# Kernel optimization log

Measured on AMD Instinct MI355X. Metric: run time of the kernel, lower is better.

Reference implementation:

```python
import jax, jax.numpy as jnp
import numpy as np

B, N, E, D_IN, D_ENC, D_GNN, D_FC, N_CLS = 16, 5000, 160000, 128, 256, 256, 128, 2


def setup_inputs() -> dict:
    key = jax.random.key(0)
    ks = jax.random.split(key, 16)
    sc = lambda d: 1.0 / np.sqrt(d)
    x = jax.random.normal(ks[0], (B, N, D_IN), dtype=jnp.float32)
    edge_index = jax.random.randint(ks[1], (B, 2, E), 0, N, dtype=jnp.int64)
    return {
        "x": x,
        "edge_index": edge_index,
        "We": jax.random.normal(ks[2], (D_IN, D_ENC), jnp.float32) * sc(D_IN),
        "be": jnp.zeros((D_ENC,), jnp.float32),
        "Wl1": jax.random.normal(ks[3], (D_ENC, D_ENC), jnp.float32) * sc(D_ENC),
        "bl1": jnp.zeros((D_ENC,), jnp.float32),
        "Wr1": jax.random.normal(ks[4], (D_ENC, D_ENC), jnp.float32) * sc(D_ENC),
        "Wl2": jax.random.normal(ks[5], (D_ENC, D_GNN), jnp.float32) * sc(D_ENC),
        "bl2": jnp.zeros((D_GNN,), jnp.float32),
        "Wr2": jax.random.normal(ks[6], (D_ENC, D_GNN), jnp.float32) * sc(D_ENC),
        "Wlp": jax.random.normal(ks[7], (D_ENC, 1), jnp.float32) * sc(D_ENC),
        "blp": jnp.zeros((1,), jnp.float32),
        "Wrp": jax.random.normal(ks[8], (D_ENC, 1), jnp.float32) * sc(D_ENC),
        "Wc1": jax.random.normal(ks[9], (D_GNN, D_FC), jnp.float32) * sc(D_GNN),
        "bc1": jnp.zeros((D_FC,), jnp.float32),
        "Wc2": jax.random.normal(ks[10], (D_FC, N_CLS), jnp.float32) * sc(D_FC),
        "bc2": jnp.zeros((N_CLS,), jnp.float32),
    }


def _sage(x, src, dst, Wl, bl, Wr):
    # PyG SAGEConv (mean aggr): lin_l(mean_{j in N(i)} x_j) + lin_r(x_i)
    agg = jax.ops.segment_sum(x[src], dst, num_segments=N)            # [N, d]
    deg = jax.ops.segment_sum(jnp.ones((src.shape[0], 1), x.dtype), dst, num_segments=N)
    mean = agg / jnp.maximum(deg, 1.0)
    return mean @ Wl + bl + x @ Wr


def reference(x, edge_index, We, be, Wl1, bl1, Wr1, Wl2, bl2, Wr2,
              Wlp, blp, Wrp, Wc1, bc1, Wc2, bc2):
    def one_bag(xb, eib):
        src, dst = eib[0], eib[1]
        h = jax.nn.relu(xb @ We + be)                                  # encoder -> [N, d_enc]
        # GNNConvStack (raw_last=False: activation after every layer)
        g = jax.nn.relu(_sage(h, src, dst, Wl1, bl1, Wr1))
        g = jax.nn.relu(_sage(g, src, dst, Wl2, bl2, Wr2))             # [N, d_gnn]
        # pooling SAGEConv on encoder output, softmax over nodes (dim=0)
        cw = jax.nn.softmax(_sage(h, src, dst, Wlp, blp, Wrp), axis=0) # [N, 1]
        # dense_diff_pool re-softmaxes s over clusters (dim=-1); with 1 cluster -> ones
        s = jax.nn.softmax(cw, axis=-1)                                # [N, 1]
        emb = (s.T @ g)[0]                                             # [d_gnn]
        # classifier (raw_last=True)
        h1 = jax.nn.relu(emb @ Wc1 + bc1)
        return h1 @ Wc2 + bc2                                          # [n_classes]

    return jax.vmap(one_bag)(x, edge_index)                           # [B, n_classes]
```

## Files before the change

### kernel.cpp

```cpp
#include <hip/hip_runtime.h>
#include <hip/hip_bf16.h>
#include <cstdint>
#include <cstddef>

#define NBAGS  16
#define NNODES 5000
#define NEDGES 160000
#define DIN    128
#define DENC   256
#define DFC    128
#define NCLS   2

#define TPB 40
#define HB  32
#define HEPB (NEDGES / HB)

typedef __attribute__((ext_vector_type(8))) short short8;
typedef __attribute__((ext_vector_type(4))) float f32x4;

static __device__ __forceinline__ ushort f2b(float v) {
    __hip_bfloat16 b = __float2bfloat16(v);
    return *reinterpret_cast<ushort*>(&b);
}

template<bool DUAL, bool RELU, bool REDUCE>
__global__ __launch_bounds__(256)
void gemm_bf16_kernel(const ushort* __restrict__ A1, const ushort* __restrict__ Wt1,
                      const ushort* __restrict__ A2, const ushort* __restrict__ Wt2,
                      const float* __restrict__ bias, ushort* __restrict__ C,
                      float* __restrict__ emb, int K)
{
    constexpr int LDSP = 40;
    __shared__ __align__(16) ushort As[128 * LDSP];
    __shared__ __align__(16) ushort Bs[128 * LDSP];

    const int bx   = blockIdx.x;
    const int bag  = bx & 15;
    const int rem  = bx >> 4;
    const int col  = rem & 1;
    const int tile = rem >> 1;
    const size_t bagRow0 = (size_t)bag * NNODES;
    const int rloc0 = tile * 128;
    const int n0 = col * 128;

    const int tid  = threadIdx.x;
    const int wave = tid >> 6;
    const int lane = tid & 63;
    const int quad = lane >> 4;
    const int l16  = lane & 15;
    const int wm   = (wave >> 1) * 64;
    const int wn   = (wave & 1) * 64;

    f32x4 acc[4][4];
#pragma unroll
    for (int i = 0; i < 4; ++i)
#pragma unroll
        for (int j = 0; j < 4; ++j)
#pragma unroll
            for (int r = 0; r < 4; ++r) acc[i][j][r] = 0.f;

    const int sr = tid >> 1;
    const int sk = (tid & 1) * 16;

    const int npass = DUAL ? 2 : 1;
    for (int pass = 0; pass < npass; ++pass) {
        const ushort* __restrict__ A = (DUAL && pass) ? A2 : A1;
        const ushort* __restrict__ W = (DUAL && pass) ? Wt2 : Wt1;

        for (int k0 = 0; k0 < K; k0 += 32) {
            {
                uint4 v0 = make_uint4(0, 0, 0, 0), v1 = make_uint4(0, 0, 0, 0);
                const int rl = rloc0 + sr;
                if (rl < NNODES) {
                    const uint4* src = (const uint4*)(A + (bagRow0 + rl) * K + k0 + sk);
                    v0 = src[0]; v1 = src[1];
                }
                *(uint4*)&As[sr * LDSP + sk]     = v0;
                *(uint4*)&As[sr * LDSP + sk + 8] = v1;
            }
            {
                const uint4* src = (const uint4*)(W + (size_t)(n0 + sr) * K + k0 + sk);
                *(uint4*)&Bs[sr * LDSP + sk]     = src[0];
                *(uint4*)&Bs[sr * LDSP + sk + 8] = src[1];
            }
            __syncthreads();

            short8 af[4], bf[4];
#pragma unroll
            for (int t = 0; t < 4; ++t) {
                af[t] = *(const short8*)&As[(wm + t * 16 + l16) * LDSP + quad * 8];
                bf[t] = *(const short8*)&Bs[(wn + t * 16 + l16) * LDSP + quad * 8];
            }
#pragma unroll
            for (int tm = 0; tm < 4; ++tm)
#pragma unroll
                for (int tn = 0; tn < 4; ++tn)
                    acc[tm][tn] = __builtin_amdgcn_mfma_f32_16x16x32_bf16(
                        af[tm], bf[tn], acc[tm][tn], 0, 0, 0);
            __syncthreads();
        }
    }

    if (!REDUCE) {
#pragma unroll
        for (int tm = 0; tm < 4; ++tm) {
            const int rbase = rloc0 + wm + tm * 16 + quad * 4;
#pragma unroll
            for (int reg = 0; reg < 4; ++reg) {
                const int rl = rbase + reg;
                if (rl < NNODES) {
#pragma unroll
                    for (int tn = 0; tn < 4; ++tn) {
                        const int gcol = n0 + wn + tn * 16 + l16;
                        float v = acc[tm][tn][reg] + bias[gcol];
                        if (RELU) v = fmaxf(v, 0.f);
                        C[(bagRow0 + rl) * 256 + gcol] = f2b(v);
                    }
                }
            }
        }
    } else {
        __shared__ float red[128];
        if (tid < 128) red[tid] = 0.f;
        __syncthreads();
#pragma unroll
        for (int tn = 0; tn < 4; ++tn) {
            const int cl = wn + tn * 16 + l16;
            const float bv = bias[n0 + cl];
            float p = 0.f;
#pragma unroll
            for (int tm = 0; tm < 4; ++tm) {
#pragma unroll
                for (int reg = 0; reg < 4; ++reg) {
                    const int rl = rloc0 + wm + tm * 16 + quad * 4 + reg;
                    float v = acc[tm][tn][reg] + bv;
                    if (RELU) v = fmaxf(v, 0.f);
                    if (rl < NNODES) p += v;
                }
            }
            atomicAdd(&red[cl], p);
        }
        __syncthreads();
        if (tid < 128)
            atomicAdd(&emb[bag * DENC + n0 + tid], red[tid]);
    }
}

__global__ __launch_bounds__(256)
void wt_transpose_kernel(const float* __restrict__ W, ushort* __restrict__ Wt, int K)
{
    const int idx = blockIdx.x * 256 + threadIdx.x;
    if (idx < 256 * K) {
        const int n = idx / K;
        const int k = idx - n * K;
        Wt[idx] = f2b(W[k * 256 + n]);
    }
}

__global__ __launch_bounds__(256)
void cvt_bf16_kernel(const float* __restrict__ x, ushort* __restrict__ xb)
{
    const int bag = blockIdx.x & 15;
    const int chunk = blockIdx.x >> 4;
    const size_t base = (size_t)bag * (NNODES * DIN / 4);
    const int i = chunk * 256 + threadIdx.x;
    const float4 v = ((const float4*)x)[base + i];
    ushort4 o;
    o.x = f2b(v.x); o.y = f2b(v.y); o.z = f2b(v.z); o.w = f2b(v.w);
    ((ushort4*)xb)[base + i] = o;
}

__global__ __launch_bounds__(256)
void hist_kernel(const int* __restrict__ edges, int* __restrict__ histG)
{
    const int bag = blockIdx.x & 15;
    const int blk = blockIdx.x >> 4;
    __shared__ int h[NNODES];
    for (int i = threadIdx.x; i < NNODES; i += 256) h[i] = 0;
    __syncthreads();
    const int* __restrict__ dstp = edges + (size_t)bag * 2 * NEDGES + NEDGES + blk * HEPB;
    for (int r = threadIdx.x; r < HEPB; r += 256)
        atomicAdd(&h[__builtin_nontemporal_load(&dstp[r])], 1);
    __syncthreads();
    int* __restrict__ out = histG + ((size_t)bag * HB + blk) * NNODES;
    for (int i = threadIdx.x; i < NNODES; i += 256) out[i] = h[i];
}

__global__ __launch_bounds__(256)
void colsum_kernel(int* __restrict__ histG, int* __restrict__ cnt)
{
    const int bag = blockIdx.x & 15;
    const int chunk = blockIdx.x >> 4;
    const int node = chunk * 256 + threadIdx.x;
    if (node >= NNODES) return;
    int* __restrict__ hb = histG + (size_t)bag * HB * NNODES + node;
    int run = 0;
#pragma unroll 8
    for (int blk = 0; blk < HB; ++blk) {
        int* p = hb + blk * NNODES;
        const int v = *p;
        *p = run;
        run += v;
    }
    cnt[bag * NNODES + node] = run;
}

__global__ __launch_bounds__(1024)
void scan_kernel(const int* __restrict__ cnt, int* __restrict__ rowptr)
{
    const int b = blockIdx.x;
    const int t = threadIdx.x;
    __shared__ int sh[1024];
    const int CH = 5;
    const int base = t * CH;
    int local[CH];
    int sum = 0;
#pragma unroll
    for (int i = 0; i < CH; ++i) {
        const int g = base + i;
        const int v = (g < NNODES) ? cnt[b * NNODES + g] : 0;
        local[i] = v; sum += v;
    }
    sh[t] = sum;
    __syncthreads();
    for (int off = 1; off < 1024; off <<= 1) {
        const int add = (t >= off) ? sh[t - off] : 0;
        __syncthreads();
        sh[t] += add;
        __syncthreads();
    }
    int run = sh[t] - sum;
#pragma unroll
    for (int i = 0; i < CH; ++i) {
        const int g = base + i;
        if (g < NNODES) rowptr[b * (NNODES + 1) + g] = run;
        run += local[i];
    }
    if (t == 1023) rowptr[b * (NNODES + 1) + NNODES] = run;
}

__global__ __launch_bounds__(256)
void place_kernel(const int* __restrict__ edges, const int* __restrict__ histG,
                  const int* __restrict__ rowptr, ushort* __restrict__ colidx)
{
    const int bag = blockIdx.x & 15;
    const int blk = blockIdx.x >> 4;
    __shared__ int h[NNODES];
    const int* __restrict__ rel = histG + ((size_t)bag * HB + blk) * NNODES;
    const int* __restrict__ rp  = rowptr + bag * (NNODES + 1);
    for (int i = threadIdx.x; i < NNODES; i += 256) h[i] = rp[i] + rel[i];
    __syncthreads();
    const int* __restrict__ eb = edges + (size_t)bag * 2 * NEDGES;
    ushort* __restrict__ co = colidx + (size_t)bag * NEDGES;
    const int e0 = blk * HEPB;
    for (int r = threadIdx.x; r < HEPB; r += 256) {
        const int s = __builtin_nontemporal_load(&eb[e0 + r]);
        const int d = __builtin_nontemporal_load(&eb[NEDGES + e0 + r]);
        const int pos = atomicAdd(&h[d], 1);
        co[pos] = (ushort)s;
    }
}

__global__ __launch_bounds__(256)
void agg_mean_kernel(const ushort* __restrict__ X, const int* __restrict__ rowptr,
                     const ushort* __restrict__ colidx, ushort* __restrict__ M,
                     int batchBase)
{
    const int bx = blockIdx.x;
    const int bag = batchBase + (bx & 7);
    const int grp = bx >> 3;
    const int wave = threadIdx.x >> 6;
    const int lane = threadIdx.x & 63;
    const int node = grp * 4 + wave;

    const int* rp = rowptr + bag * (NNODES + 1);
    const int s = rp[node];
    const int e = rp[node + 1];
    const float inv = 1.0f / fmaxf((float)(e - s), 1.0f);
    const uint2* __restrict__ Xb = (const uint2*)(X + (size_t)bag * NNODES * DENC);
    const ushort* __restrict__ ci = colidx + (size_t)bag * NEDGES;

    float2 p0 = {0.f, 0.f}, p1 = {0.f, 0.f};
    int j = s;
    for (; j + 4 <= e; j += 4) {
        const int i0 = ci[j], i1 = ci[j + 1], i2 = ci[j + 2], i3 = ci[j + 3];
        const uint2 u0 = Xb[i0 * 64 + lane];
        const uint2 u1 = Xb[i1 * 64 + lane];
        const uint2 u2 = Xb[i2 * 64 + lane];
        const uint2 u3 = Xb[i3 * 64 + lane];
        p0.x += __uint_as_float(u0.x << 16); p0.y += __uint_as_float(u0.x & 0xffff0000u);
        p1.x += __uint_as_float(u0.y << 16); p1.y += __uint_as_float(u0.y & 0xffff0000u);
        p0.x += __uint_as_float(u1.x << 16); p0.y += __uint_as_float(u1.x & 0xffff0000u);
        p1.x += __uint_as_float(u1.y << 16); p1.y += __uint_as_float(u1.y & 0xffff0000u);
        p0.x += __uint_as_float(u2.x << 16); p0.y += __uint_as_float(u2.x & 0xffff0000u);
        p1.x += __uint_as_float(u2.y << 16); p1.y += __uint_as_float(u2.y & 0xffff0000u);
        p0.x += __uint_as_float(u3.x << 16); p0.y += __uint_as_float(u3.x & 0xffff0000u);
        p1.x += __uint_as_float(u3.y << 16); p1.y += __uint_as_float(u3.y & 0xffff0000u);
    }
    for (; j < e; ++j) {
        const uint2 u = Xb[ci[j] * 64 + lane];
        p0.x += __uint_as_float(u.x << 16); p0.y += __uint_as_float(u.x & 0xffff0000u);
        p1.x += __uint_as_float(u.y << 16); p1.y += __uint_as_float(u.y & 0xffff0000u);
    }
    const uint32_t w0 = (uint32_t)f2b(p0.x * inv) | ((uint32_t)f2b(p0.y * inv) << 16);
    const uint32_t w1 = (uint32_t)f2b(p1.x * inv) | ((uint32_t)f2b(p1.y * inv) << 16);
    const uint64_t o = (uint64_t)w0 | ((uint64_t)w1 << 32);
    uint64_t* dst = (uint64_t*)(M + ((size_t)bag * NNODES + node) * DENC) + lane;
    __builtin_nontemporal_store(o, dst);
}

__global__ __launch_bounds__(128)
void classifier_kernel(const float* __restrict__ emb, const float* __restrict__ Wc1,
                       const float* __restrict__ bc1, const float* __restrict__ Wc2,
                       const float* __restrict__ bc2, float* __restrict__ out)
{
    const int b = blockIdx.x;
    const int t = threadIdx.x;
    __shared__ float se[DENC];
    se[t] = emb[b * DENC + t];
    se[128 + t] = emb[b * DENC + 128 + t];
    __syncthreads();
    float h = bc1[t];
    for (int k = 0; k < DENC; ++k) h = fmaf(se[k], Wc1[k * DFC + t], h);
    h = fmaxf(h, 0.f);
    __shared__ float s0[128], s1[128];
    s0[t] = h * Wc2[t * NCLS + 0];
    s1[t] = h * Wc2[t * NCLS + 1];
    __syncthreads();
    for (int off = 64; off > 0; off >>= 1) {
        if (t < off) { s0[t] += s0[t + off]; s1[t] += s1[t + off]; }
        __syncthreads();
    }
    if (t == 0) {
        out[b * NCLS + 0] = s0[0] + bc2[0];
        out[b * NCLS + 1] = s1[0] + bc2[1];
    }
}

extern "C" void kernel_launch(void* const* d_in, const int* in_sizes, int n_in,
                              void* d_out, int out_size, void* d_ws, size_t ws_size,
                              hipStream_t stream)
{
    const float* x    = (const float*)d_in[0];
    const int*   edges= (const int*)d_in[1];
    const float* We   = (const float*)d_in[2];
    const float* be   = (const float*)d_in[3];
    const float* Wl1  = (const float*)d_in[4];
    const float* bl1  = (const float*)d_in[5];
    const float* Wr1  = (const float*)d_in[6];
    const float* Wl2  = (const float*)d_in[7];
    const float* bl2  = (const float*)d_in[8];
    const float* Wr2  = (const float*)d_in[9];
    const float* Wc1  = (const float*)d_in[13];
    const float* bc1  = (const float*)d_in[14];
    const float* Wc2  = (const float*)d_in[15];
    const float* bc2  = (const float*)d_in[16];
    float* out = (float*)d_out;

    auto rnd = [](size_t v) { return (v + 255) & ~(size_t)255; };
    char* p = (char*)d_ws;
    auto alloc = [&](size_t bytes) -> char* {
        char* r = p; p += rnd(bytes); return r;
    };
    ushort* xb    = (ushort*)alloc((size_t)NBAGS * NNODES * DIN * 2);
    ushort* H     = (ushort*)alloc((size_t)NBAGS * NNODES * DENC * 2);
    ushort* Mb    = (ushort*)alloc((size_t)NBAGS * NNODES * DENC * 2);
    ushort* Gb    = (ushort*)alloc((size_t)NBAGS * NNODES * DENC * 2);
    ushort* Wet   = (ushort*)alloc((size_t)256 * DIN * 2);
    ushort* Wl1t  = (ushort*)alloc((size_t)256 * DENC * 2);
    ushort* Wr1t  = (ushort*)alloc((size_t)256 * DENC * 2);
    ushort* Wl2t  = (ushort*)alloc((size_t)256 * DENC * 2);
    ushort* Wr2t  = (ushort*)alloc((size_t)256 * DENC * 2);
    int*    rowptr= (int*)   alloc((size_t)NBAGS * (NNODES + 1) * 4);
    int*    cnt   = (int*)   alloc((size_t)NBAGS * NNODES * 4);
    int*    histG = (int*)   alloc((size_t)NBAGS * HB * NNODES * 4);
    ushort* colidx= (ushort*)alloc((size_t)NBAGS * NEDGES * 2);
    float*  emb   = (float*) alloc((size_t)NBAGS * DENC * 4);

    (void)hipMemsetAsync(emb, 0, (size_t)NBAGS * DENC * 4, stream);

    cvt_bf16_kernel<<<NBAGS * 625, 256, 0, stream>>>(x, xb);
    wt_transpose_kernel<<<(256 * DIN + 255) / 256, 256, 0, stream>>>(We, Wet, DIN);
    wt_transpose_kernel<<<(256 * DENC + 255) / 256, 256, 0, stream>>>(Wl1, Wl1t, DENC);
    wt_transpose_kernel<<<(256 * DENC + 255) / 256, 256, 0, stream>>>(Wr1, Wr1t, DENC);
    wt_transpose_kernel<<<(256 * DENC + 255) / 256, 256, 0, stream>>>(Wl2, Wl2t, DENC);
    wt_transpose_kernel<<<(256 * DENC + 255) / 256, 256, 0, stream>>>(Wr2, Wr2t, DENC);

    hist_kernel<<<NBAGS * HB, 256, 0, stream>>>(edges, histG);
    colsum_kernel<<<NBAGS * 20, 256, 0, stream>>>(histG, cnt);
    scan_kernel<<<NBAGS, 1024, 0, stream>>>(cnt, rowptr);
    place_kernel<<<NBAGS * HB, 256, 0, stream>>>(edges, histG, rowptr, colidx);

    const int gemm_grid = NBAGS * TPB * 2;
    const int agg_grid  = 8 * (NNODES / 4);

    gemm_bf16_kernel<false, true, false><<<gemm_grid, 256, 0, stream>>>(
        xb, Wet, nullptr, nullptr, be, H, nullptr, DIN);

    agg_mean_kernel<<<agg_grid, 256, 0, stream>>>(H, rowptr, colidx, Mb, 0);
    agg_mean_kernel<<<agg_grid, 256, 0, stream>>>(H, rowptr, colidx, Mb, 8);
    gemm_bf16_kernel<true, true, false><<<gemm_grid, 256, 0, stream>>>(
        Mb, Wl1t, H, Wr1t, bl1, Gb, nullptr, DENC);

    agg_mean_kernel<<<agg_grid, 256, 0, stream>>>(Gb, rowptr, colidx, H, 0);
    agg_mean_kernel<<<agg_grid, 256, 0, stream>>>(Gb, rowptr, colidx, H, 8);
    gemm_bf16_kernel<true, true, true><<<gemm_grid, 256, 0, stream>>>(
        H, Wl2t, Gb, Wr2t, bl2, nullptr, emb, DENC);

    classifier_kernel<<<NBAGS, 128, 0, stream>>>(emb, Wc1, bc1, Wc2, bc2, out);
}
```

Measured before the change: 513.8 us.

## Merge prep kernels, co-launch encoder GEMM with edge placement, widen aggregation loads

```diff
diff --git a/kernel.cpp b/kernel.cpp
--- a/kernel.cpp
+++ b/kernel.cpp
@@ -14,9 +14,11 @@
 #define TPB 40
 #define HB  32
 #define HEPB (NEDGES / HB)
+#define LDSP 40
 
 typedef __attribute__((ext_vector_type(8))) short short8;
 typedef __attribute__((ext_vector_type(4))) float f32x4;
+typedef unsigned int uint32x4 __attribute__((ext_vector_type(4)));
 
 static __device__ __forceinline__ ushort f2b(float v) {
     __hip_bfloat16 b = __float2bfloat16(v);
@@ -24,17 +26,16 @@
 }
 
 template<bool DUAL, bool RELU, bool REDUCE>
-__global__ __launch_bounds__(256)
-void gemm_bf16_kernel(const ushort* __restrict__ A1, const ushort* __restrict__ Wt1,
-                      const ushort* __restrict__ A2, const ushort* __restrict__ Wt2,
-                      const float* __restrict__ bias, ushort* __restrict__ C,
-                      float* __restrict__ emb, int K)
-{
-    constexpr int LDSP = 40;
-    __shared__ __align__(16) ushort As[128 * LDSP];
-    __shared__ __align__(16) ushort Bs[128 * LDSP];
-
-    const int bx   = blockIdx.x;
+__device__ __forceinline__
+void gemm_body(int bx, char* smem,
+               const ushort* __restrict__ A1, const ushort* __restrict__ Wt1,
+               const ushort* __restrict__ A2, const ushort* __restrict__ Wt2,
+               const float* __restrict__ bias, ushort* __restrict__ C,
+               float* __restrict__ emb, int K)
+{
+    ushort* As = (ushort*)smem;
+    ushort* Bs = As + 128 * LDSP;
+
     const int bag  = bx & 15;
     const int rem  = bx >> 4;
     const int col  = rem & 1;
@@ -120,7 +121,7 @@
             }
         }
     } else {
-        __shared__ float red[128];
+        float* red = (float*)smem;
         if (tid < 128) red[tid] = 0.f;
         __syncthreads();
 #pragma unroll
@@ -146,44 +147,108 @@
     }
 }
 
+template<bool DUAL, bool RELU, bool REDUCE>
 __global__ __launch_bounds__(256)
-void wt_transpose_kernel(const float* __restrict__ W, ushort* __restrict__ Wt, int K)
-{
-    const int idx = blockIdx.x * 256 + threadIdx.x;
-    if (idx < 256 * K) {
-        const int n = idx / K;
-        const int k = idx - n * K;
+void gemm_bf16_kernel(const ushort* __restrict__ A1, const ushort* __restrict__ Wt1,
+                      const ushort* __restrict__ A2, const ushort* __restrict__ Wt2,
+                      const float* __restrict__ bias, ushort* __restrict__ C,
+                      float* __restrict__ emb, int K)
+{
+    __shared__ __align__(16) char smem[2 * 128 * LDSP * 2];
+    gemm_body<DUAL, RELU, REDUCE>(blockIdx.x, smem, A1, Wt1, A2, Wt2, bias, C, emb, K);
+}
+
+__device__ __forceinline__
+void place_body(int pbx, char* smem, const int* __restrict__ edges,
+                const int* __restrict__ histG, const int* __restrict__ rowptr,
+                ushort* __restrict__ colidx)
+{
+    const int bag = pbx & 15;
+    const int blk = pbx >> 4;
+    int* h = (int*)smem;
+    const int* __restrict__ rel = histG + ((size_t)bag * HB + blk) * NNODES;
+    const int* __restrict__ rp  = rowptr + bag * (NNODES + 1);
+    for (int i = threadIdx.x; i < NNODES; i += 256) h[i] = rp[i] + rel[i];
+    __syncthreads();
+    const int* __restrict__ eb = edges + (size_t)bag * 2 * NEDGES;
+    ushort* __restrict__ co = colidx + (size_t)bag * NEDGES;
+    const int e0 = blk * HEPB;
+    for (int r = threadIdx.x; r < HEPB; r += 256) {
+        const int s = __builtin_nontemporal_load(&eb[e0 + r]);
+        const int d = __builtin_nontemporal_load(&eb[NEDGES + e0 + r]);
+        const int pos = atomicAdd(&h[d], 1);
+        co[pos] = (ushort)s;
+    }
+}
+
+__global__ __launch_bounds__(256)
+void enc_place_kernel(const ushort* __restrict__ xb, const ushort* __restrict__ Wet,
+                      const float* __restrict__ be, ushort* __restrict__ H,
+                      const int* __restrict__ edges, const int* __restrict__ histG,
+                      const int* __restrict__ rowptr, ushort* __restrict__ colidx)
+{
+    __shared__ __align__(16) char smem[2 * 128 * LDSP * 2];
+    if (blockIdx.x < NBAGS * TPB * 2)
+        gemm_body<false, true, false>(blockIdx.x, smem, xb, Wet, nullptr, nullptr,
+                                      be, H, nullptr, DIN);
+    else
+        place_body(blockIdx.x - NBAGS * TPB * 2, smem, edges, histG, rowptr, colidx);
+}
+
+#define HIST_B (NBAGS * HB)
+#define CVT_B  (NBAGS * 625)
+#define WTE_B  128
+#define WTW_B  1024
+#define PREP_GRID (HIST_B + CVT_B + WTE_B + WTW_B)
+
+__global__ __launch_bounds__(256)
+void prep_kernel(const int* __restrict__ edges, int* __restrict__ histG,
+                 const float* __restrict__ x, ushort* __restrict__ xb,
+                 const float* __restrict__ We,  ushort* __restrict__ Wet,
+                 const float* __restrict__ Wl1, ushort* __restrict__ Wl1t,
+                 const float* __restrict__ Wr1, ushort* __restrict__ Wr1t,
+                 const float* __restrict__ Wl2, ushort* __restrict__ Wl2t,
+                 const float* __restrict__ Wr2, ushort* __restrict__ Wr2t)
+{
+    __shared__ int sh[NNODES];
+    const int bx = blockIdx.x;
+    if (bx < HIST_B) {
+        const int bag = bx & 15;
+        const int blk = bx >> 4;
+        for (int i = threadIdx.x; i < NNODES; i += 256) sh[i] = 0;
+        __syncthreads();
+        const int* __restrict__ dstp =
+            edges + (size_t)bag * 2 * NEDGES + NEDGES + blk * HEPB;
+        for (int r = threadIdx.x; r < HEPB; r += 256)
+            atomicAdd(&sh[__builtin_nontemporal_load(&dstp[r])], 1);
+        __syncthreads();
+        int* __restrict__ out = histG + ((size_t)bag * HB + blk) * NNODES;
+        for (int i = threadIdx.x; i < NNODES; i += 256) out[i] = sh[i];
+    } else if (bx < HIST_B + CVT_B) {
+        const int cbx = bx - HIST_B;
+        const int bag = cbx & 15;
+        const int chunk = cbx >> 4;
+        const size_t base = (size_t)bag * (NNODES * DIN / 4);
+        const int i = chunk * 256 + threadIdx.x;
+        const float4 v = ((const float4*)x)[base + i];
+        ushort4 o;
+        o.x = f2b(v.x); o.y = f2b(v.y); o.z = f2b(v.z); o.w = f2b(v.w);
+        ((ushort4*)xb)[base + i] = o;
+    } else if (bx < HIST_B + CVT_B + WTE_B) {
+        const int idx = (bx - HIST_B - CVT_B) * 256 + threadIdx.x;
+        const int n = idx / DIN;
+        const int k = idx - n * DIN;
+        Wet[idx] = f2b(We[k * 256 + n]);
+    } else {
+        const int r = bx - HIST_B - CVT_B - WTE_B;
+        const int which = r >> 8;
+        const int idx = (r & 255) * 256 + threadIdx.x;
+        const int n = idx >> 8;
+        const int k = idx & 255;
+        const float* W  = (which == 0) ? Wl1 : (which == 1) ? Wr1 : (which == 2) ? Wl2 : Wr2;
+        ushort* Wt      = (which == 0) ? Wl1t : (which == 1) ? Wr1t : (which == 2) ? Wl2t : Wr2t;
         Wt[idx] = f2b(W[k * 256 + n]);
     }
-}
-
-__global__ __launch_bounds__(256)
-void cvt_bf16_kernel(const float* __restrict__ x, ushort* __restrict__ xb)
-{
-    const int bag = blockIdx.x & 15;
-    const int chunk = blockIdx.x >> 4;
-    const size_t base = (size_t)bag * (NNODES * DIN / 4);
-    const int i = chunk * 256 + threadIdx.x;
-    const float4 v = ((const float4*)x)[base + i];
-    ushort4 o;
-    o.x = f2b(v.x); o.y = f2b(v.y); o.z = f2b(v.z); o.w = f2b(v.w);
-    ((ushort4*)xb)[base + i] = o;
-}
-
-__global__ __launch_bounds__(256)
-void hist_kernel(const int* __restrict__ edges, int* __restrict__ histG)
-{
-    const int bag = blockIdx.x & 15;
-    const int blk = blockIdx.x >> 4;
-    __shared__ int h[NNODES];
-    for (int i = threadIdx.x; i < NNODES; i += 256) h[i] = 0;
-    __syncthreads();
-    const int* __restrict__ dstp = edges + (size_t)bag * 2 * NEDGES + NEDGES + blk * HEPB;
-    for (int r = threadIdx.x; r < HEPB; r += 256)
-        atomicAdd(&h[__builtin_nontemporal_load(&dstp[r])], 1);
-    __syncthreads();
-    int* __restrict__ out = histG + ((size_t)bag * HB + blk) * NNODES;
-    for (int i = threadIdx.x; i < NNODES; i += 256) out[i] = h[i];
 }
 
 __global__ __launch_bounds__(256)
@@ -240,28 +305,6 @@
 }
 
 __global__ __launch_bounds__(256)
-void place_kernel(const int* __restrict__ edges, const int* __restrict__ histG,
-                  const int* __restrict__ rowptr, ushort* __restrict__ colidx)
-{
-    const int bag = blockIdx.x & 15;
-    const int blk = blockIdx.x >> 4;
-    __shared__ int h[NNODES];
-    const int* __restrict__ rel = histG + ((size_t)bag * HB + blk) * NNODES;
-    const int* __restrict__ rp  = rowptr + bag * (NNODES + 1);
-    for (int i = threadIdx.x; i < NNODES; i += 256) h[i] = rp[i] + rel[i];
-    __syncthreads();
-    const int* __restrict__ eb = edges + (size_t)bag * 2 * NEDGES;
-    ushort* __restrict__ co = colidx + (size_t)bag * NEDGES;
-    const int e0 = blk * HEPB;
-    for (int r = threadIdx.x; r < HEPB; r += 256) {
-        const int s = __builtin_nontemporal_load(&eb[e0 + r]);
-        const int d = __builtin_nontemporal_load(&eb[NEDGES + e0 + r]);
-        const int pos = atomicAdd(&h[d], 1);
-        co[pos] = (ushort)s;
-    }
-}
-
-__global__ __launch_bounds__(256)
 void agg_mean_kernel(const ushort* __restrict__ X, const int* __restrict__ rowptr,
                      const ushort* __restrict__ colidx, ushort* __restrict__ M,
                      int batchBase)
@@ -271,42 +314,67 @@
     const int grp = bx >> 3;
     const int wave = threadIdx.x >> 6;
     const int lane = threadIdx.x & 63;
+    const int half = lane >> 5;
+    const int hl = lane & 31;
     const int node = grp * 4 + wave;
 
     const int* rp = rowptr + bag * (NNODES + 1);
     const int s = rp[node];
     const int e = rp[node + 1];
     const float inv = 1.0f / fmaxf((float)(e - s), 1.0f);
-    const uint2* __restrict__ Xb = (const uint2*)(X + (size_t)bag * NNODES * DENC);
+    const uint32x4* __restrict__ Xb = (const uint32x4*)(X + (size_t)bag * NNODES * DENC);
     const ushort* __restrict__ ci = colidx + (size_t)bag * NEDGES;
 
-    float2 p0 = {0.f, 0.f}, p1 = {0.f, 0.f};
+    float2 a0 = {0.f, 0.f}, a1 = {0.f, 0.f}, a2 = {0.f, 0.f}, a3 = {0.f, 0.f};
+
     int j = s;
-    for (; j + 4 <= e; j += 4) {
-        const int i0 = ci[j], i1 = ci[j + 1], i2 = ci[j + 2], i3 = ci[j + 3];
-        const uint2 u0 = Xb[i0 * 64 + lane];
-        const uint2 u1 = Xb[i1 * 64 + lane];
-        const uint2 u2 = Xb[i2 * 64 + lane];
-        const uint2 u3 = Xb[i3 * 64 + lane];
-        p0.x += __uint_as_float(u0.x << 16); p0.y += __uint_as_float(u0.x & 0xffff0000u);
-        p1.x += __uint_as_float(u0.y << 16); p1.y += __uint_as_float(u0.y & 0xffff0000u);
-        p0.x += __uint_as_float(u1.x << 16); p0.y += __uint_as_float(u1.x & 0xffff0000u);
-        p1.x += __uint_as_float(u1.y << 16); p1.y += __uint_as_float(u1.y & 0xffff0000u);
-        p0.x += __uint_as_float(u2.x << 16); p0.y += __uint_as_float(u2.x & 0xffff0000u);
-        p1.x += __uint_as_float(u2.y << 16); p1.y += __uint_as_float(u2.y & 0xffff0000u);
-        p0.x += __uint_as_float(u3.x << 16); p0.y += __uint_as_float(u3.x & 0xffff0000u);
-        p1.x += __uint_as_float(u3.y << 16); p1.y += __uint_as_float(u3.y & 0xffff0000u);
-    }
-    for (; j < e; ++j) {
-        const uint2 u = Xb[ci[j] * 64 + lane];
-        p0.x += __uint_as_float(u.x << 16); p0.y += __uint_as_float(u.x & 0xffff0000u);
-        p1.x += __uint_as_float(u.y << 16); p1.y += __uint_as_float(u.y & 0xffff0000u);
-    }
-    const uint32_t w0 = (uint32_t)f2b(p0.x * inv) | ((uint32_t)f2b(p0.y * inv) << 16);
-    const uint32_t w1 = (uint32_t)f2b(p1.x * inv) | ((uint32_t)f2b(p1.y * inv) << 16);
-    const uint64_t o = (uint64_t)w0 | ((uint64_t)w1 << 32);
-    uint64_t* dst = (uint64_t*)(M + ((size_t)bag * NNODES + node) * DENC) + lane;
-    __builtin_nontemporal_store(o, dst);
+    for (; j + 8 <= e; j += 8) {
+        int idx[4];
+#pragma unroll
+        for (int t = 0; t < 4; ++t) idx[t] = ci[j + 2 * t + half];
+        uint32x4 u[4];
+#pragma unroll
+        for (int t = 0; t < 4; ++t) u[t] = Xb[idx[t] * 32 + hl];
+#pragma unroll
+        for (int t = 0; t < 4; ++t) {
+            a0.x += __uint_as_float(u[t].x << 16);
+            a0.y += __uint_as_float(u[t].x & 0xffff0000u);
+            a1.x += __uint_as_float(u[t].y << 16);
+            a1.y += __uint_as_float(u[t].y & 0xffff0000u);
+            a2.x += __uint_as_float(u[t].z << 16);
+            a2.y += __uint_as_float(u[t].z & 0xffff0000u);
+            a3.x += __uint_as_float(u[t].w << 16);
+            a3.y += __uint_as_float(u[t].w & 0xffff0000u);
+        }
+    }
+    for (; j < e; j += 2) {
+        const int jj = j + half;
+        uint32x4 u = {0u, 0u, 0u, 0u};
+        if (jj < e) u = Xb[(int)ci[jj] * 32 + hl];
+        a0.x += __uint_as_float(u.x << 16);
+        a0.y += __uint_as_float(u.x & 0xffff0000u);
+        a1.x += __uint_as_float(u.y << 16);
+        a1.y += __uint_as_float(u.y & 0xffff0000u);
+        a2.x += __uint_as_float(u.z << 16);
+        a2.y += __uint_as_float(u.z & 0xffff0000u);
+        a3.x += __uint_as_float(u.w << 16);
+        a3.y += __uint_as_float(u.w & 0xffff0000u);
+    }
+
+    a0.x += __shfl_xor(a0.x, 32); a0.y += __shfl_xor(a0.y, 32);
+    a1.x += __shfl_xor(a1.x, 32); a1.y += __shfl_xor(a1.y, 32);
+    a2.x += __shfl_xor(a2.x, 32); a2.y += __shfl_xor(a2.y, 32);
+    a3.x += __shfl_xor(a3.x, 32); a3.y += __shfl_xor(a3.y, 32);
+
+    if (half == 0) {
+        uint32x4 o;
+        o.x = (uint32_t)f2b(a0.x * inv) | ((uint32_t)f2b(a0.y * inv) << 16);
+        o.y = (uint32_t)f2b(a1.x * inv) | ((uint32_t)f2b(a1.y * inv) << 16);
+        o.z = (uint32_t)f2b(a2.x * inv) | ((uint32_t)f2b(a2.y * inv) << 16);
+        o.w = (uint32_t)f2b(a3.x * inv) | ((uint32_t)f2b(a3.y * inv) << 16);
+        uint32x4* dst = (uint32x4*)(M + ((size_t)bag * NNODES + node) * DENC) + hl;
+        __builtin_nontemporal_store(o, dst);
+    }
 }
 
 __global__ __launch_bounds__(128)
@@ -379,23 +447,17 @@
 
     (void)hipMemsetAsync(emb, 0, (size_t)NBAGS * DENC * 4, stream);
 
-    cvt_bf16_kernel<<<NBAGS * 625, 256, 0, stream>>>(x, xb);
-    wt_transpose_kernel<<<(256 * DIN + 255) / 256, 256, 0, stream>>>(We, Wet, DIN);
-    wt_transpose_kernel<<<(256 * DENC + 255) / 256, 256, 0, stream>>>(Wl1, Wl1t, DENC);
-    wt_transpose_kernel<<<(256 * DENC + 255) / 256, 256, 0, stream>>>(Wr1, Wr1t, DENC);
-    wt_transpose_kernel<<<(256 * DENC + 255) / 256, 256, 0, stream>>>(Wl2, Wl2t, DENC);
-    wt_transpose_kernel<<<(256 * DENC + 255) / 256, 256, 0, stream>>>(Wr2, Wr2t, DENC);
-
-    hist_kernel<<<NBAGS * HB, 256, 0, stream>>>(edges, histG);
+    prep_kernel<<<PREP_GRID, 256, 0, stream>>>(
+        edges, histG, x, xb, We, Wet, Wl1, Wl1t, Wr1, Wr1t, Wl2, Wl2t, Wr2, Wr2t);
+
     colsum_kernel<<<NBAGS * 20, 256, 0, stream>>>(histG, cnt);
     scan_kernel<<<NBAGS, 1024, 0, stream>>>(cnt, rowptr);
-    place_kernel<<<NBAGS * HB, 256, 0, stream>>>(edges, histG, rowptr, colidx);
+
+    enc_place_kernel<<<NBAGS * TPB * 2 + HIST_B, 256, 0, stream>>>(
+        xb, Wet, be, H, edges, histG, rowptr, colidx);
 
     const int gemm_grid = NBAGS * TPB * 2;
     const int agg_grid  = 8 * (NNODES / 4);
-
-    gemm_bf16_kernel<false, true, false><<<gemm_grid, 256, 0, stream>>>(
-        xb, Wet, nullptr, nullptr, be, H, nullptr, DIN);
 
     agg_mean_kernel<<<agg_grid, 256, 0, stream>>>(H, rowptr, colidx, Mb, 0);
     agg_mean_kernel<<<agg_grid, 256, 0, stream>>>(H, rowptr, colidx, Mb, 8);
```

New measurement: 413.1 us. 19.6% less time.
